# Optimization experiments

Hardware: AMD Instinct MI355X
Metric: run time of the kernel (lower is better)

## Reference

```python
import jax, jax.numpy as jnp
import numpy as np

N, H, B, E = 8192, 64, 8, 262144


def setup_inputs() -> dict:
    key = jax.random.key(0)
    ks = jax.random.split(key, 16)
    inp = {
        "x": jax.random.uniform(ks[0], (B, N, 2), dtype=jnp.float32),
        "edge_index": jax.random.randint(ks[1], (2, E), 0, N, dtype=jnp.int64),
        "target_node": jax.random.randint(ks[2], (B,), 0, N, dtype=jnp.int64),
        "current_prereq_mask": jax.random.uniform(ks[3], (B, N), dtype=jnp.float32),
        # learned parameters (eval mode: dropout is identity)
        "node_emb": jax.random.normal(ks[4], (N, H), dtype=jnp.float32) * 0.02,
        "W_sp": jax.random.normal(ks[5], (H, 2), dtype=jnp.float32) * 0.5,
        "b_sp": jnp.zeros((H,), dtype=jnp.float32),
        "W_g": jax.random.normal(ks[6], (H, H), dtype=jnp.float32) * (1.0 / np.sqrt(H)),
        "b_g": jnp.zeros((H,), dtype=jnp.float32),
        "W_d": jax.random.normal(ks[7], (1, H), dtype=jnp.float32) * (1.0 / np.sqrt(H)),
        "b_d": jnp.zeros((1,), dtype=jnp.float32),
        "W_a": jax.random.normal(ks[8], (1, H), dtype=jnp.float32) * (1.0 / np.sqrt(H)),
        "b_a": jnp.zeros((1,), dtype=jnp.float32),
        "prereq_w": jnp.array([1.0], dtype=jnp.float32),
    }
    return inp


def _build_adj_norm(edge_index):
    # A_hat = A + I ; adj_norm = D^{-1/2} A_hat D^{-1/2}, dense [N, N]
    adj = jnp.zeros((N, N), dtype=jnp.float32).at[edge_index[0], edge_index[1]].set(1.0)
    adj = adj + jnp.eye(N, dtype=jnp.float32)
    deg = adj.sum(axis=1)
    dis = jnp.where(deg > 0, deg ** -0.5, 0.0)
    return dis[:, None] * adj * dis[None, :]


def reference(x, edge_index, target_node, current_prereq_mask,
              node_emb, W_sp, b_sp, W_g, b_g, W_d, b_d, W_a, b_a, prereq_w):
    adj_norm = _build_adj_norm(edge_index)               # [N, N]
    h = node_emb[None] + x @ W_sp.T + b_sp               # [B, N, H]
    h_proj = h @ W_g.T                                   # [B, N, H]
    z = jnp.einsum('nm,bmh->bnh', adj_norm, h_proj) + b_g
    z = jax.nn.relu(z)                                   # [B, N, H]

    target_emb = jnp.take_along_axis(z, target_node[:, None, None].astype(jnp.int32).repeat(1, axis=1), axis=1)[:, 0, :]  # [B, H]
    difficulty = (target_emb @ W_d.T + b_d)[:, 0]        # [B]

    scores = x[:, :, 1]                                  # [B, N]
    n_learned = jnp.clip(x[:, :, 0].sum(axis=1), 1.0)    # [B]
    weighted_z = jnp.einsum('bnh,bn->bh', z, scores) / n_learned[:, None]
    ability = (weighted_z @ W_a.T + b_a)[:, 0]           # [B]

    z_pos = jax.nn.softplus(z)
    prereq_agg = jnp.einsum('bnh,bn->bh', z_pos, current_prereq_mask).mean(axis=-1)  # [B]
    prereq_strength = jnp.abs(prereq_w)[0] * prereq_agg

    gap = ability - difficulty + prereq_strength
    prob = jax.nn.sigmoid(gap)
    return prob, gap
```

## Files before the change

### kernel.cpp

```cpp
#include <hip/hip_runtime.h>
#include <hip/hip_fp16.h>
#include <math.h>

#define N 8192
#define H 64
#define B 8
#define MAXDEG 128
#define REPS 16

#define OFF_CNT  0ULL
#define OFF_WR   32768ULL
#define OFF_PR   65536ULL
#define OFF_NLR  98304ULL
#define ZERO_END 98816ULL
#define OFF_COLS 98816ULL
#define OFF_TGT  2195968ULL
#define OFF_UV   2198016ULL
#define OFF_REC  2198784ULL

__global__ __launch_bounds__(256) void k_zero(float4* __restrict__ p) {
    unsigned i = blockIdx.x * 256u + threadIdx.x;
    if (i < (unsigned)(ZERO_END / 16))
        p[i] = make_float4(0.f, 0.f, 0.f, 0.f);
}

__global__ __launch_bounds__(256) void k_edges(const int* __restrict__ ei, int nE,
                                               unsigned* __restrict__ cnt,
                                               unsigned short* __restrict__ cols) {
    int e = blockIdx.x * 256 + threadIdx.x;
    if (e >= nE) return;
    int r = ei[e];
    int c = ei[nE + e];
    unsigned k = atomicAdd(&cnt[r], 1u);
    if (k < MAXDEG) cols[r * MAXDEG + k] = (unsigned short)c;
}

__global__ __launch_bounds__(256) void k_prep(const float* __restrict__ ne,
                                              const float* __restrict__ W_g,
                                              const float* __restrict__ W_sp,
                                              const float* __restrict__ b_sp,
                                              const float* __restrict__ x,
                                              const float* __restrict__ pmask,
                                              unsigned* __restrict__ cnt,
                                              unsigned short* __restrict__ cols,
                                              unsigned* __restrict__ rec,
                                              float* __restrict__ uvec) {
    __shared__ float wgs[H * 65];
    __shared__ unsigned short ls[4][MAXDEG];
    const int tid = threadIdx.x, lane = tid & 63, wv = tid >> 6;
    const int bid = blockIdx.x;

    for (int e = tid; e < H * H; e += 256)
        wgs[(e >> 6) * 65 + (e & 63)] = W_g[e];
    __syncthreads();

    float wr[H];
#pragma unroll
    for (int k = 0; k < H; ++k) wr[k] = wgs[lane * 65 + k];

    if (bid == 0 && wv == 0) {
        float v0 = W_sp[lane * 2 + 0], v1 = W_sp[lane * 2 + 1], vb = b_sp[lane];
        float a0 = 0.f, a1 = 0.f, a2 = 0.f;
#pragma unroll
        for (int k = 0; k < H; ++k) {
            a0 = fmaf(wr[k], __shfl(v0, k, 64), a0);
            a1 = fmaf(wr[k], __shfl(v1, k, 64), a1);
            a2 = fmaf(wr[k], __shfl(vb, k, 64), a2);
        }
        uvec[lane] = a0; uvec[64 + lane] = a1; uvec[128 + lane] = a2;
    }

    for (int i = 0; i < 2; ++i) {
        const int r = (bid * 4 + wv) * 2 + i;
        const int kraw = min((int)cnt[r], MAXDEG);
        unsigned short* cl = &cols[r * MAXDEG];
        for (int t = lane; t < kraw; t += 64) ls[wv][t] = cl[t];
        int c0 = (lane < kraw) ? (int)ls[wv][lane] : -1;
        int dup0 = 0;
        for (int j = 0; j < lane && j < kraw; ++j)
            dup0 |= ((int)ls[wv][j] == c0);
        unsigned long long m0 = __ballot((lane < kraw) && !dup0);
        unsigned long long below = (1ULL << lane) - 1ULL;
        unsigned tot = __popcll(m0);
        if ((lane < kraw) && !dup0)
            cl[__popcll(m0 & below)] = (unsigned short)c0;
        if (kraw > 64) {
            const int i1 = lane + 64;
            int c1 = (i1 < kraw) ? (int)ls[wv][i1] : -2;
            int dup1 = 0;
            for (int j = 0; j < i1 && j < kraw; ++j)
                dup1 |= ((int)ls[wv][j] == c1);
            unsigned long long m1 = __ballot((i1 < kraw) && !dup1);
            if ((i1 < kraw) && !dup1)
                cl[tot + __popcll(m1 & below)] = (unsigned short)c1;
            tot += __popcll(m1);
        }
        if (lane == 0) cnt[r] = tot;
        const float dis = rsqrtf((float)(tot + 1u));

        float xvx = 0.f, xvy = 0.f, pm = 0.f;
        if (lane < 8) {
            float2 t2 = ((const float2*)x)[lane * N + r];
            xvx = t2.x; xvy = t2.y;
        }
        if (lane >= 17 && lane < 25) pm = pmask[(lane - 17) * N + r];
        float yv = __shfl(xvy, lane & 7, 64);
        float aux = (lane < 8)   ? dis * xvx
                  : (lane < 16)  ? dis * yv
                  : (lane == 16) ? dis
                  : (lane < 25)  ? pm : 0.f;

        const float4* ne4 = (const float4*)(ne + (size_t)r * H);
        float acc = 0.f;
#pragma unroll
        for (int kk = 0; kk < 16; ++kk) {
            float4 h4 = ne4[kk];
            acc = fmaf(wr[4 * kk + 0], h4.x, acc);
            acc = fmaf(wr[4 * kk + 1], h4.y, acc);
            acc = fmaf(wr[4 * kk + 2], h4.z, acc);
            acc = fmaf(wr[4 * kk + 3], h4.w, acc);
        }
        unsigned w = ((unsigned)__half_as_ushort(__float2half(dis * acc)) << 16)
                   |  (unsigned)__half_as_ushort(__float2half(aux));
        rec[(size_t)r * 64 + lane] = w;
    }
}

__global__ __launch_bounds__(256) void k_spmm(const unsigned* __restrict__ rec,
                                              const unsigned* __restrict__ cnt,
                                              const unsigned short* __restrict__ cols,
                                              const float* __restrict__ uvec,
                                              const float* __restrict__ b_g,
                                              const int* __restrict__ target,
                                              float* __restrict__ wr_,
                                              float* __restrict__ pr_,
                                              float* __restrict__ nlr,
                                              float* __restrict__ tgt) {
    const int lane = threadIdx.x & 63, wv = threadIdx.x >> 6;
    const int r = blockIdx.x * 4 + wv;
    const float u0 = uvec[lane], u1 = uvec[64 + lane], ub = uvec[128 + lane];
    const float bg = b_g[lane];
    int tg[B];
#pragma unroll
    for (int b = 0; b < B; ++b) tg[b] = target[b];

    const unsigned vown = rec[(size_t)r * 64 + lane];
    float2 fown = __half22float2(*(const __half2*)&vown);

    float spA = fown.y, sxA = fown.x, spB = 0.f, sxB = 0.f;
    const int kc = min((int)cnt[r], MAXDEG);
    const unsigned short* cl = &cols[r * MAXDEG];
    int k = 0;
#pragma unroll 2
    for (; k + 2 <= kc; k += 2) {
        int cA = cl[k], cB = cl[k + 1];
        unsigned vA = rec[(size_t)cA * 64 + lane];
        unsigned vB = rec[(size_t)cB * 64 + lane];
        float2 fA = __half22float2(*(const __half2*)&vA);
        float2 fB = __half22float2(*(const __half2*)&vB);
        spA += fA.y; sxA += fA.x;
        spB += fB.y; sxB += fB.x;
    }
    if (k < kc) {
        int c = cl[k];
        unsigned v = rec[(size_t)c * 64 + lane];
        float2 f = __half22float2(*(const __half2*)&v);
        spA += f.y; sxA += f.x;
    }
    const float sp = spA + spB;
    const float sx = sxA + sxB;

    const float dis_r = __shfl(fown.x, 16, 64);
    const float rdis = 1.0f / dis_r;
    const float sd = __shfl(sx, 16, 64);
    const float base = fmaf(sd, ub, sp);
    float wa[B], pa[B];
#pragma unroll
    for (int b = 0; b < B; ++b) {
        float sx0 = __shfl(sx, b, 64);
        float sx1 = __shfl(sx, 8 + b, 64);
        float sc  = __shfl(fown.x, 8 + b, 64) * rdis;
        float mk  = __shfl(fown.x, 17 + b, 64);
        float v = fmaf(sx0, u0, fmaf(sx1, u1, base));
        float z = fmaxf(fmaf(dis_r, v, bg), 0.f);
        wa[b] = z * sc;
        pa[b] = (z + __logf(1.f + __expf(-z))) * mk;
        if (r == tg[b]) tgt[b * H + lane] = z;
    }
    const int rep = r & (REPS - 1);
#pragma unroll
    for (int b = 0; b < B; ++b) {
        atomicAdd(&wr_[(rep * B + b) * H + lane], wa[b]);
        atomicAdd(&pr_[(rep * B + b) * H + lane], pa[b]);
    }
    if (lane < 8) atomicAdd(&nlr[rep * 8 + lane], fown.x * rdis);
}

__global__ __launch_bounds__(512) void k_final(const float* __restrict__ wr_,
                                               const float* __restrict__ pr_,
                                               const float* __restrict__ nlr,
                                               const float* __restrict__ tgt,
                                               const float* __restrict__ W_d,
                                               const float* __restrict__ b_d,
                                               const float* __restrict__ W_a,
                                               const float* __restrict__ b_a,
                                               const float* __restrict__ prereq_w,
                                               float* __restrict__ out) {
    int tid = threadIdx.x, b = tid >> 6, h = tid & 63;
    float ws = 0.f, ps = 0.f, nlv = 0.f;
#pragma unroll
    for (int rep = 0; rep < REPS; ++rep) {
        ws  += wr_[(rep * B + b) * H + h];
        ps  += pr_[(rep * B + b) * H + h];
        nlv += nlr[rep * 8 + b];
    }
    float nl = fmaxf(nlv, 1.0f);
    float ap = (ws / nl) * W_a[h];
    float dp = tgt[b * H + h] * W_d[h];
    float pp = ps;
    for (int off = 32; off; off >>= 1) {
        ap += __shfl_down(ap, off, 64);
        dp += __shfl_down(dp, off, 64);
        pp += __shfl_down(pp, off, 64);
    }
    if (h == 0) {
        float ability    = ap + b_a[0];
        float difficulty = dp + b_d[0];
        float preq       = fabsf(prereq_w[0]) * (pp * (1.0f / (float)H));
        float gap  = ability - difficulty + preq;
        float prob = 1.0f / (1.0f + __expf(-gap));
        out[b]     = prob;
        out[B + b] = gap;
    }
}

extern "C" void kernel_launch(void* const* d_in, const int* in_sizes, int n_in,
                              void* d_out, int out_size, void* d_ws, size_t ws_size,
                              hipStream_t stream) {
    const float* x        = (const float*)d_in[0];
    const int*   ei       = (const int*)d_in[1];
    const int*   target   = (const int*)d_in[2];
    const float* pmask    = (const float*)d_in[3];
    const float* ne       = (const float*)d_in[4];
    const float* W_sp     = (const float*)d_in[5];
    const float* b_sp     = (const float*)d_in[6];
    const float* W_g      = (const float*)d_in[7];
    const float* b_g      = (const float*)d_in[8];
    const float* W_d      = (const float*)d_in[9];
    const float* b_d      = (const float*)d_in[10];
    const float* W_a      = (const float*)d_in[11];
    const float* b_a      = (const float*)d_in[12];
    const float* prereq_w = (const float*)d_in[13];

    const int nE = in_sizes[1] / 2;

    char* ws = (char*)d_ws;
    unsigned*        cnt  = (unsigned*)(ws + OFF_CNT);
    float*           wr_  = (float*)(ws + OFF_WR);
    float*           pr_  = (float*)(ws + OFF_PR);
    float*           nlr  = (float*)(ws + OFF_NLR);
    unsigned short*  cols = (unsigned short*)(ws + OFF_COLS);
    float*           tgt  = (float*)(ws + OFF_TGT);
    float*           uvec = (float*)(ws + OFF_UV);
    unsigned*        rec  = (unsigned*)(ws + OFF_REC);

    k_zero<<<(unsigned)(ZERO_END / 16 + 255) / 256, 256, 0, stream>>>((float4*)ws);
    k_edges<<<(nE + 255) / 256, 256, 0, stream>>>(ei, nE, cnt, cols);
    k_prep<<<N / 8, 256, 0, stream>>>(ne, W_g, W_sp, b_sp, x, pmask, cnt, cols,
                                      rec, uvec);
    k_spmm<<<N / 4, 256, 0, stream>>>(rec, cnt, cols, uvec, b_g, target,
                                      wr_, pr_, nlr, tgt);
    k_final<<<1, 512, 0, stream>>>(wr_, pr_, nlr, tgt, W_d, b_d, W_a, b_a,
                                   prereq_w, (float*)d_out);
}
```

Before: 93.51 us.

## Reduce SpMM partial sums in shared memory before global atomics; shuffle column indices

The SpMM kernel now uses 1024-thread blocks (16 rows each) and accumulates the per-batch weighted and prereq sums in LDS atomics. Each block then issues one global atomic per element into 8 replica slots instead of 16, which cuts global atomic traffic by roughly 16x. Column indices are loaded once per wave into a register and broadcast with shuffles, replacing repeated scalar loads. Risks are LDS atomic contention among 16 waves and the extra barrier; rows with more than 64 neighbours fall back to direct loads.

```diff
diff --git a/kernel.cpp b/kernel.cpp
--- a/kernel.cpp
+++ b/kernel.cpp
@@ -6,17 +6,17 @@
 #define H 64
 #define B 8
 #define MAXDEG 128
-#define REPS 16
+#define REPS 8
 
 #define OFF_CNT  0ULL
 #define OFF_WR   32768ULL
-#define OFF_PR   65536ULL
-#define OFF_NLR  98304ULL
-#define ZERO_END 98816ULL
-#define OFF_COLS 98816ULL
-#define OFF_TGT  2195968ULL
-#define OFF_UV   2198016ULL
-#define OFF_REC  2198784ULL
+#define OFF_PR   49152ULL
+#define OFF_NLR  65536ULL
+#define ZERO_END 65792ULL
+#define OFF_COLS 65792ULL
+#define OFF_TGT  2162944ULL
+#define OFF_UV   2164992ULL
+#define OFF_REC  2165760ULL
 
 __global__ __launch_bounds__(256) void k_zero(float4* __restrict__ p) {
     unsigned i = blockIdx.x * 256u + threadIdx.x;
@@ -126,18 +126,27 @@
     }
 }
 
-__global__ __launch_bounds__(256) void k_spmm(const unsigned* __restrict__ rec,
-                                              const unsigned* __restrict__ cnt,
-                                              const unsigned short* __restrict__ cols,
-                                              const float* __restrict__ uvec,
-                                              const float* __restrict__ b_g,
-                                              const int* __restrict__ target,
-                                              float* __restrict__ wr_,
-                                              float* __restrict__ pr_,
-                                              float* __restrict__ nlr,
-                                              float* __restrict__ tgt) {
-    const int lane = threadIdx.x & 63, wv = threadIdx.x >> 6;
-    const int r = blockIdx.x * 4 + wv;
+__global__ __launch_bounds__(1024, 2) void k_spmm(const unsigned* __restrict__ rec,
+                                                  const unsigned* __restrict__ cnt,
+                                                  const unsigned short* __restrict__ cols,
+                                                  const float* __restrict__ uvec,
+                                                  const float* __restrict__ b_g,
+                                                  const int* __restrict__ target,
+                                                  float* __restrict__ wr_,
+                                                  float* __restrict__ pr_,
+                                                  float* __restrict__ nlr,
+                                                  float* __restrict__ tgt) {
+    __shared__ float lw[B * H];
+    __shared__ float lp[B * H];
+    __shared__ float lnl[B];
+    const int tid = threadIdx.x;
+    const int lane = tid & 63, wv = tid >> 6;
+    const int r = blockIdx.x * 16 + wv;
+
+    if (tid < B * H) { lw[tid] = 0.f; lp[tid] = 0.f; }
+    if (tid < B) lnl[tid] = 0.f;
+    __syncthreads();
+
     const float u0 = uvec[lane], u1 = uvec[64 + lane], ub = uvec[128 + lane];
     const float bg = b_g[lane];
     int tg[B];
@@ -147,13 +156,16 @@
     const unsigned vown = rec[(size_t)r * 64 + lane];
     float2 fown = __half22float2(*(const __half2*)&vown);
 
-    float spA = fown.y, sxA = fown.x, spB = 0.f, sxB = 0.f;
     const int kc = min((int)cnt[r], MAXDEG);
     const unsigned short* cl = &cols[r * MAXDEG];
+    int creg = (lane < kc) ? (int)cl[lane] : 0;
+
+    float spA = fown.y, sxA = fown.x, spB = 0.f, sxB = 0.f;
+    const int kc64 = min(kc, 64);
     int k = 0;
-#pragma unroll 2
-    for (; k + 2 <= kc; k += 2) {
-        int cA = cl[k], cB = cl[k + 1];
+    for (; k + 2 <= kc64; k += 2) {
+        int cA = __shfl(creg, k, 64);
+        int cB = __shfl(creg, k + 1, 64);
         unsigned vA = rec[(size_t)cA * 64 + lane];
         unsigned vB = rec[(size_t)cB * 64 + lane];
         float2 fA = __half22float2(*(const __half2*)&vA);
@@ -161,8 +173,14 @@
         spA += fA.y; sxA += fA.x;
         spB += fB.y; sxB += fB.x;
     }
-    if (k < kc) {
-        int c = cl[k];
+    if (k < kc64) {
+        int c = __shfl(creg, k, 64);
+        unsigned v = rec[(size_t)c * 64 + lane];
+        float2 f = __half22float2(*(const __half2*)&v);
+        spA += f.y; sxA += f.x;
+    }
+    for (int kk = 64; kk < kc; ++kk) {
+        int c = (int)cl[kk];
         unsigned v = rec[(size_t)c * 64 + lane];
         float2 f = __half22float2(*(const __half2*)&v);
         spA += f.y; sxA += f.x;
@@ -174,7 +192,6 @@
     const float rdis = 1.0f / dis_r;
     const float sd = __shfl(sx, 16, 64);
     const float base = fmaf(sd, ub, sp);
-    float wa[B], pa[B];
 #pragma unroll
     for (int b = 0; b < B; ++b) {
         float sx0 = __shfl(sx, b, 64);
@@ -183,17 +200,17 @@
         float mk  = __shfl(fown.x, 17 + b, 64);
         float v = fmaf(sx0, u0, fmaf(sx1, u1, base));
         float z = fmaxf(fmaf(dis_r, v, bg), 0.f);
-        wa[b] = z * sc;
-        pa[b] = (z + __logf(1.f + __expf(-z))) * mk;
+        atomicAdd(&lw[b * H + lane], z * sc);
+        atomicAdd(&lp[b * H + lane], (z + __logf(1.f + __expf(-z))) * mk);
         if (r == tg[b]) tgt[b * H + lane] = z;
     }
-    const int rep = r & (REPS - 1);
-#pragma unroll
-    for (int b = 0; b < B; ++b) {
-        atomicAdd(&wr_[(rep * B + b) * H + lane], wa[b]);
-        atomicAdd(&pr_[(rep * B + b) * H + lane], pa[b]);
-    }
-    if (lane < 8) atomicAdd(&nlr[rep * 8 + lane], fown.x * rdis);
+    if (lane < 8) atomicAdd(&lnl[lane], fown.x * rdis);
+    __syncthreads();
+
+    const int rep = blockIdx.x & (REPS - 1);
+    if (tid < B * H)           atomicAdd(&wr_[rep * B * H + tid], lw[tid]);
+    else if (tid < 2 * B * H)  atomicAdd(&pr_[rep * B * H + tid - B * H], lp[tid - B * H]);
+    if (tid < B)               atomicAdd(&nlr[rep * B + tid], lnl[tid]);
 }
 
 __global__ __launch_bounds__(512) void k_final(const float* __restrict__ wr_,
@@ -212,7 +229,7 @@
     for (int rep = 0; rep < REPS; ++rep) {
         ws  += wr_[(rep * B + b) * H + h];
         ps  += pr_[(rep * B + b) * H + h];
-        nlv += nlr[rep * 8 + b];
+        nlv += nlr[rep * B + b];
     }
     float nl = fmaxf(nlv, 1.0f);
     float ap = (ws / nl) * W_a[h];
@@ -268,8 +285,8 @@
     k_edges<<<(nE + 255) / 256, 256, 0, stream>>>(ei, nE, cnt, cols);
     k_prep<<<N / 8, 256, 0, stream>>>(ne, W_g, W_sp, b_sp, x, pmask, cnt, cols,
                                       rec, uvec);
-    k_spmm<<<N / 4, 256, 0, stream>>>(rec, cnt, cols, uvec, b_g, target,
-                                      wr_, pr_, nlr, tgt);
+    k_spmm<<<N / 16, 1024, 0, stream>>>(rec, cnt, cols, uvec, b_g, target,
+                                        wr_, pr_, nlr, tgt);
     k_final<<<1, 512, 0, stream>>>(wr_, pr_, nlr, tgt, W_d, b_d, W_a, b_a,
                                    prereq_w, (float*)d_out);
 }
```

After: 89.92 us. -3.8%, faster.

## Stream node records through LDS tiles and sort neighbor lists for tiled SpMM

Applied to the files above, without the earlier changes.

Neighbor column lists are now sorted in k_prep with a wave-level bitonic sort, covering the first 64 entries. k_spmm becomes a 1024-thread block handling 32 rows. It streams all of rec through shared memory in 256-row tiles and accumulates each row's sorted neighbors from the tile, instead of gathering them at random from global memory. Per-block LDS atomics reduce the batch outputs before one global atomic per element. The cost is that every block reads the whole 2 MB rec array, which is much more total traffic than the sparse gather, and it syncs the block twice per tile.

```diff
diff --git a/kernel.cpp b/kernel.cpp
--- a/kernel.cpp
+++ b/kernel.cpp
@@ -7,6 +7,8 @@
 #define B 8
 #define MAXDEG 128
 #define REPS 16
+#define TILE 256
+#define NPH  (N / TILE)
 
 #define OFF_CNT  0ULL
 #define OFF_WR   32768ULL
@@ -33,6 +35,22 @@
     int c = ei[nE + e];
     unsigned k = atomicAdd(&cnt[r], 1u);
     if (k < MAXDEG) cols[r * MAXDEG + k] = (unsigned short)c;
+}
+
+__device__ __forceinline__ int bitonic64(int v, int lane) {
+#pragma unroll
+    for (int k = 2; k <= 64; k <<= 1) {
+#pragma unroll
+        for (int j = k >> 1; j >= 1; j >>= 1) {
+            int other = __shfl_xor(v, j, 64);
+            bool lower = (lane & j) == 0;
+            bool up = (lane & k) == 0;
+            bool keepMin = (lower == up);
+            int mn = min(v, other), mx = max(v, other);
+            v = keepMin ? mn : mx;
+        }
+    }
+    return v;
 }
 
 __global__ __launch_bounds__(256) void k_prep(const float* __restrict__ ne,
@@ -82,9 +100,13 @@
         unsigned long long m0 = __ballot((lane < kraw) && !dup0);
         unsigned long long below = (1ULL << lane) - 1ULL;
         unsigned tot = __popcll(m0);
-        if ((lane < kraw) && !dup0)
-            cl[__popcll(m0 & below)] = (unsigned short)c0;
-        if (kraw > 64) {
+        if (kraw <= 64) {
+            int sv = ((lane < kraw) && !dup0) ? c0 : N;
+            sv = bitonic64(sv, lane);
+            cl[lane] = (unsigned short)sv;
+        } else {
+            if ((lane < kraw) && !dup0)
+                cl[__popcll(m0 & below)] = (unsigned short)c0;
             const int i1 = lane + 64;
             int c1 = (i1 < kraw) ? (int)ls[wv][i1] : -2;
             int dup1 = 0;
@@ -94,6 +116,9 @@
             if ((i1 < kraw) && !dup1)
                 cl[tot + __popcll(m1 & below)] = (unsigned short)c1;
             tot += __popcll(m1);
+            int sv = (lane < (int)min(tot, 64u)) ? (int)cl[lane] : N;
+            sv = bitonic64(sv, lane);
+            cl[lane] = (unsigned short)sv;
         }
         if (lane == 0) cnt[r] = tot;
         const float dis = rsqrtf((float)(tot + 1u));
@@ -126,74 +151,116 @@
     }
 }
 
-__global__ __launch_bounds__(256) void k_spmm(const unsigned* __restrict__ rec,
-                                              const unsigned* __restrict__ cnt,
-                                              const unsigned short* __restrict__ cols,
-                                              const float* __restrict__ uvec,
-                                              const float* __restrict__ b_g,
-                                              const int* __restrict__ target,
-                                              float* __restrict__ wr_,
-                                              float* __restrict__ pr_,
-                                              float* __restrict__ nlr,
-                                              float* __restrict__ tgt) {
-    const int lane = threadIdx.x & 63, wv = threadIdx.x >> 6;
-    const int r = blockIdx.x * 4 + wv;
+__global__ __launch_bounds__(1024) void k_spmm(const unsigned* __restrict__ rec,
+                                               const unsigned* __restrict__ cnt,
+                                               const unsigned short* __restrict__ cols,
+                                               const float* __restrict__ uvec,
+                                               const float* __restrict__ b_g,
+                                               const int* __restrict__ target,
+                                               float* __restrict__ wr_,
+                                               float* __restrict__ pr_,
+                                               float* __restrict__ nlr,
+                                               float* __restrict__ tgt) {
+    __shared__ unsigned tile[TILE * 64];
+    const int tid = threadIdx.x;
+    const int lane = tid & 63, wv = tid >> 6;
+    const int r0 = blockIdx.x * 32 + wv * 2;
+    const int r1 = r0 + 1;
+
     const float u0 = uvec[lane], u1 = uvec[64 + lane], ub = uvec[128 + lane];
     const float bg = b_g[lane];
     int tg[B];
 #pragma unroll
     for (int b = 0; b < B; ++b) tg[b] = target[b];
 
-    const unsigned vown = rec[(size_t)r * 64 + lane];
-    float2 fown = __half22float2(*(const __half2*)&vown);
-
-    float spA = fown.y, sxA = fown.x, spB = 0.f, sxB = 0.f;
-    const int kc = min((int)cnt[r], MAXDEG);
-    const unsigned short* cl = &cols[r * MAXDEG];
-    int k = 0;
-#pragma unroll 2
-    for (; k + 2 <= kc; k += 2) {
-        int cA = cl[k], cB = cl[k + 1];
-        unsigned vA = rec[(size_t)cA * 64 + lane];
-        unsigned vB = rec[(size_t)cB * 64 + lane];
-        float2 fA = __half22float2(*(const __half2*)&vA);
-        float2 fB = __half22float2(*(const __half2*)&vB);
-        spA += fA.y; sxA += fA.x;
-        spB += fB.y; sxB += fB.x;
-    }
-    if (k < kc) {
-        int c = cl[k];
-        unsigned v = rec[(size_t)c * 64 + lane];
+    unsigned v0_ = rec[(size_t)r0 * 64 + lane];
+    unsigned v1_ = rec[(size_t)r1 * 64 + lane];
+    float2 f0 = __half22float2(*(const __half2*)&v0_);
+    float2 f1 = __half22float2(*(const __half2*)&v1_);
+    float sp0 = f0.y, sx0 = f0.x, sp1 = f1.y, sx1 = f1.x;
+    const int kc0 = min((int)cnt[r0], MAXDEG);
+    const int kc1 = min((int)cnt[r1], MAXDEG);
+    const int creg0 = (int)cols[r0 * MAXDEG + lane];
+    const int creg1 = (int)cols[r1 * MAXDEG + lane];
+    int kp0 = 0, kp1 = 0;
+
+    for (int t = 0; t < NPH; ++t) {
+        const int base = t * TILE, tend = base + TILE;
+        __syncthreads();
+        {
+            const uint4* src = (const uint4*)(rec + (size_t)base * 64);
+            uint4* dst = (uint4*)tile;
+#pragma unroll
+            for (int j = 0; j < 4; ++j)
+                dst[tid + j * 1024] = src[tid + j * 1024];
+        }
+        __syncthreads();
+        while (kp0 < 64) {
+            int c = __shfl(creg0, kp0, 64);
+            if (c >= tend) break;
+            unsigned v = tile[(c - base) * 64 + lane];
+            float2 f = __half22float2(*(const __half2*)&v);
+            sp0 += f.y; sx0 += f.x; ++kp0;
+        }
+        while (kp1 < 64) {
+            int c = __shfl(creg1, kp1, 64);
+            if (c >= tend) break;
+            unsigned v = tile[(c - base) * 64 + lane];
+            float2 f = __half22float2(*(const __half2*)&v);
+            sp1 += f.y; sx1 += f.x; ++kp1;
+        }
+    }
+    for (int kk = 64; kk < kc0; ++kk) {
+        unsigned v = rec[(size_t)((int)cols[r0 * MAXDEG + kk]) * 64 + lane];
         float2 f = __half22float2(*(const __half2*)&v);
-        spA += f.y; sxA += f.x;
-    }
-    const float sp = spA + spB;
-    const float sx = sxA + sxB;
-
-    const float dis_r = __shfl(fown.x, 16, 64);
-    const float rdis = 1.0f / dis_r;
-    const float sd = __shfl(sx, 16, 64);
-    const float base = fmaf(sd, ub, sp);
-    float wa[B], pa[B];
-#pragma unroll
-    for (int b = 0; b < B; ++b) {
-        float sx0 = __shfl(sx, b, 64);
-        float sx1 = __shfl(sx, 8 + b, 64);
-        float sc  = __shfl(fown.x, 8 + b, 64) * rdis;
-        float mk  = __shfl(fown.x, 17 + b, 64);
-        float v = fmaf(sx0, u0, fmaf(sx1, u1, base));
-        float z = fmaxf(fmaf(dis_r, v, bg), 0.f);
-        wa[b] = z * sc;
-        pa[b] = (z + __logf(1.f + __expf(-z))) * mk;
-        if (r == tg[b]) tgt[b * H + lane] = z;
-    }
-    const int rep = r & (REPS - 1);
-#pragma unroll
-    for (int b = 0; b < B; ++b) {
-        atomicAdd(&wr_[(rep * B + b) * H + lane], wa[b]);
-        atomicAdd(&pr_[(rep * B + b) * H + lane], pa[b]);
-    }
-    if (lane < 8) atomicAdd(&nlr[rep * 8 + lane], fown.x * rdis);
+        sp0 += f.y; sx0 += f.x;
+    }
+    for (int kk = 64; kk < kc1; ++kk) {
+        unsigned v = rec[(size_t)((int)cols[r1 * MAXDEG + kk]) * 64 + lane];
+        float2 f = __half22float2(*(const __half2*)&v);
+        sp1 += f.y; sx1 += f.x;
+    }
+
+    __syncthreads();
+    float* lw  = (float*)tile;
+    float* lp  = lw + 512;
+    float* lnl = lp + 512;
+    if (tid < 1032) ((float*)tile)[tid] = 0.f;
+    __syncthreads();
+
+#pragma unroll
+    for (int i = 0; i < 2; ++i) {
+        const float sp = i ? sp1 : sp0;
+        const float sx = i ? sx1 : sx0;
+        const float fx = i ? f1.x : f0.x;
+        const int   r  = i ? r1 : r0;
+        const float dis_r = __shfl(fx, 16, 64);
+        const float rdis = 1.0f / dis_r;
+        const float sd = __shfl(sx, 16, 64);
+        const float base2 = fmaf(sd, ub, sp);
+#pragma unroll
+        for (int b = 0; b < B; ++b) {
+            float sa = __shfl(sx, b, 64);
+            float sb = __shfl(sx, 8 + b, 64);
+            float sc = __shfl(fx, 8 + b, 64) * rdis;
+            float mk = __shfl(fx, 17 + b, 64);
+            float v = fmaf(sa, u0, fmaf(sb, u1, base2));
+            float z = fmaxf(fmaf(dis_r, v, bg), 0.f);
+            atomicAdd(&lw[b * H + lane], z * sc);
+            atomicAdd(&lp[b * H + lane], (z + __logf(1.f + __expf(-z))) * mk);
+            if (r == tg[b]) tgt[b * H + lane] = z;
+        }
+        if (lane < 8) atomicAdd(&lnl[lane], fx * rdis);
+    }
+    __syncthreads();
+
+    const int rep = blockIdx.x & (REPS - 1);
+    if (tid < 512)           atomicAdd(&wr_[rep * 512 + tid], lw[tid]);
+    else if (tid < 1024)     atomicAdd(&pr_[rep * 512 + tid - 512], lp[tid - 512]);
+    if (tid >= 1024 - B && tid < 1024) {
+        int b = tid - (1024 - B);
+        atomicAdd(&nlr[rep * B + b], lnl[b]);
+    }
 }
 
 __global__ __launch_bounds__(512) void k_final(const float* __restrict__ wr_,
@@ -210,9 +277,9 @@
     float ws = 0.f, ps = 0.f, nlv = 0.f;
 #pragma unroll
     for (int rep = 0; rep < REPS; ++rep) {
-        ws  += wr_[(rep * B + b) * H + h];
-        ps  += pr_[(rep * B + b) * H + h];
-        nlv += nlr[rep * 8 + b];
+        ws  += wr_[rep * 512 + b * H + h];
+        ps  += pr_[rep * 512 + b * H + h];
+        nlv += nlr[rep * B + b];
     }
     float nl = fmaxf(nlv, 1.0f);
     float ap = (ws / nl) * W_a[h];
@@ -268,8 +335,8 @@
     k_edges<<<(nE + 255) / 256, 256, 0, stream>>>(ei, nE, cnt, cols);
     k_prep<<<N / 8, 256, 0, stream>>>(ne, W_g, W_sp, b_sp, x, pmask, cnt, cols,
                                       rec, uvec);
-    k_spmm<<<N / 4, 256, 0, stream>>>(rec, cnt, cols, uvec, b_g, target,
-                                      wr_, pr_, nlr, tgt);
+    k_spmm<<<N / 32, 1024, 0, stream>>>(rec, cnt, cols, uvec, b_g, target,
+                                        wr_, pr_, nlr, tgt);
     k_final<<<1, 512, 0, stream>>>(wr_, pr_, nlr, tgt, W_d, b_d, W_a, b_a,
                                    prereq_w, (float*)d_out);
 }
```

Result: slower. 139.2 us (+48.9%).
